# Optimization experiments

Hardware: AMD Instinct MI355X
Metric: run time of the kernel (lower is better)

Reference implementation:

```python
import jax, jax.numpy as jnp
import numpy as np

D_MODEL, D_K, D_V = 1024, 128, 128
B, S = 8, 2048


def setup_inputs() -> dict:
    key = jax.random.key(0)
    ks = jax.random.split(key, 10)
    scale = 1.0 / np.sqrt(D_MODEL)
    return {
        "inputs_q": jax.random.normal(ks[0], (B, S, D_MODEL), jnp.float32),
        "inputs_k": jax.random.normal(ks[1], (B, S, D_MODEL), jnp.float32),
        "inputs_v": jax.random.normal(ks[2], (B, S, D_MODEL), jnp.float32),
        "mask": jax.random.randint(ks[3], (B, 1, S), 0, 2, jnp.int32),
        "Wq": jax.random.normal(ks[4], (D_MODEL, D_K), jnp.float32) * scale,
        "bq": jnp.zeros((D_K,), jnp.float32),
        "Wk": jax.random.normal(ks[5], (D_MODEL, D_K), jnp.float32) * scale,
        "bk": jnp.zeros((D_K,), jnp.float32),
        "Wv": jax.random.normal(ks[6], (D_MODEL, D_V), jnp.float32) * scale,
        "bv": jnp.zeros((D_V,), jnp.float32),
    }


def reference(inputs_q, inputs_k, inputs_v, mask, Wq, bq, Wk, bk, Wv, bv):
    query = inputs_q @ Wq + bq            # [B,Sq,d_k]
    key = inputs_k @ Wk + bk              # [B,Sk,d_k]
    value = inputs_v @ Wv + bv            # [B,Sk,d_v]
    scores = jnp.einsum('bqd,bkd->bqk', query, key) / jnp.sqrt(jnp.float32(D_K))
    # original: mask==True means attend; inverted mask positions get -1e9
    mask_float = jnp.logical_not(mask.astype(bool)).astype(jnp.float32)  # [B,1,Sk]
    scores = scores + mask_float * (-1e9)
    attention_weights = jax.nn.softmax(scores, axis=-1)
    attention_weights = attention_weights * (1.0 - mask_float)
    output = jnp.einsum('bqk,bkv->bqv', attention_weights, value)
    return output
```

## Files before the change

kernel.cpp:

```cpp
#include <hip/hip_runtime.h>

#define L2E 1.44269504088896341f
#define SM_SHIFT 5.77078016355585f

typedef _Float16 h8 __attribute__((ext_vector_type(8)));
typedef float f4 __attribute__((ext_vector_type(4)));

__device__ __forceinline__ void gll16(const void* g, void* l) {
  __builtin_amdgcn_global_load_lds((const __attribute__((address_space(1))) void*)g,
                                   (__attribute__((address_space(3))) void*)l, 16, 0, 0);
}

__device__ __forceinline__ f4 mfma_h(h8 a, h8 b, f4 c) {
  return __builtin_amdgcn_mfma_f32_16x16x32_f16(a, b, c, 0, 0, 0);
}

__device__ __forceinline__ h8 pack8(const float4& a, const float4& b) {
  h8 hv;
  hv[0] = (_Float16)a.x; hv[1] = (_Float16)a.y; hv[2] = (_Float16)a.z; hv[3] = (_Float16)a.w;
  hv[4] = (_Float16)b.x; hv[5] = (_Float16)b.y; hv[6] = (_Float16)b.z; hv[7] = (_Float16)b.w;
  return hv;
}

__global__ void wt_prep(const float* __restrict__ Wq, const float* __restrict__ Wk,
                        const float* __restrict__ Wv, const int* __restrict__ maskp,
                        _Float16* __restrict__ Wt, _Float16* __restrict__ mh) {
  int z = blockIdx.y;
  const float* W = (z == 0) ? Wq : ((z == 1) ? Wk : Wv);
  _Float16* o = Wt + (size_t)z * 131072;
  int idx = blockIdx.x * 256 + threadIdx.x;
  int k = idx >> 7, n = idx & 127;
  o[(k >> 6) * 8192 + ((k >> 3) & 7) * 1024 + n * 8 + (k & 7)] = (_Float16)W[idx];
  if (z == 0 && idx < 16384) mh[idx] = (_Float16)(float)maskp[idx];
}

__global__ __launch_bounds__(256, 3) void proj_qkv(
    const float* __restrict__ Xq, const float* __restrict__ Xk, const float* __restrict__ Xv,
    const _Float16* __restrict__ Wt, const int* __restrict__ maskp,
    const float* __restrict__ bq, const float* __restrict__ bk, const float* __restrict__ bv,
    _Float16* __restrict__ Qh, _Float16* __restrict__ Kpk, _Float16* __restrict__ Vpk) {
  const int z = blockIdx.y;
  const float* X; const float* bias;
  if (z == 0) { X = Xq; bias = bq; }
  else if (z == 1) { X = Xk; bias = bk; }
  else { X = Xv; bias = bv; }
  const _Float16* Wz = Wt + (size_t)z * 131072;
  const int row0 = blockIdx.x * 64;
  const int tid = threadIdx.x;
  const int lane = tid & 63, wid = tid >> 6;
  const int wr = wid >> 1, wc = wid & 1;
  const int l15 = lane & 15, g = lane >> 4;

  __shared__ __align__(16) _Float16 Al[4096];
  __shared__ __align__(16) _Float16 Bl[2][8192];

  f4 acc[2][4];
#pragma unroll
  for (int i = 0; i < 2; i++)
#pragma unroll
    for (int j = 0; j < 4; j++) acc[i][j] = (f4){0.f, 0.f, 0.f, 0.f};

  float4 areg[2][2];
  const int ar_row = tid >> 3, ar_ko = tid & 7;
  auto loadA = [&](int t) {
#pragma unroll
    for (int it = 0; it < 2; it++) {
      const float* gp = X + (size_t)(row0 + it * 32 + ar_row) * 1024 + t * 64 + ar_ko * 8;
      areg[it][0] = *(const float4*)gp;
      areg[it][1] = *(const float4*)(gp + 4);
    }
  };
  auto writeA = [&]() {
#pragma unroll
    for (int it = 0; it < 2; it++) {
      int row = it * 32 + ar_row;
      *(h8*)&Al[(row * 8 + (ar_ko ^ (row & 7))) * 8] = pack8(areg[it][0], areg[it][1]);
    }
  };
  auto loadB = [&](int buf, int t) {
#pragma unroll
    for (int it = 0; it < 4; it++)
      gll16(Wz + t * 8192 + it * 2048 + tid * 8, &Bl[buf][it * 2048 + tid * 8]);
  };
  auto compute = [&](int buf) {
#pragma unroll
    for (int kc = 0; kc < 2; kc++) {
      int o = kc * 4 + g;
      h8 af[2], bf[4];
#pragma unroll
      for (int mf = 0; mf < 2; mf++) {
        int row = wr * 32 + mf * 16 + l15;
        af[mf] = *(const h8*)&Al[(row * 8 + (o ^ (row & 7))) * 8];
      }
#pragma unroll
      for (int nf = 0; nf < 4; nf++) {
        int col = wc * 64 + nf * 16 + l15;
        bf[nf] = *(const h8*)&Bl[buf][(o * 128 + col) * 8];
      }
#pragma unroll
      for (int mf = 0; mf < 2; mf++)
#pragma unroll
        for (int nf = 0; nf < 4; nf++)
          acc[mf][nf] = mfma_h(af[mf], bf[nf], acc[mf][nf]);
    }
  };

  loadA(0);
  loadB(0, 0);

  int cur = 0;
  for (int t = 0; t < 16; t++) {
    writeA();
    __syncthreads();
    if (t < 15) {
      loadA(t + 1);
      loadB(cur ^ 1, t + 1);
    }
    compute(cur);
    __syncthreads();
    cur ^= 1;
  }

  const float qscale = (z == 0) ? 0.08838834764831845f : 1.0f;
#pragma unroll
  for (int nf = 0; nf < 4; nf++) {
    int colb = wc * 64 + nf * 16 + l15;
    float bv_ = bias[colb];
#pragma unroll
    for (int mf = 0; mf < 2; mf++)
#pragma unroll
      for (int jj = 0; jj < 4; jj++) {
        int m = row0 + wr * 32 + mf * 16 + g * 4 + jj;
        float v = (acc[mf][nf][jj] + bv_) * qscale;
        if (z == 2) v *= (float)maskp[m];
        _Float16 hv = (_Float16)v;
        if (z == 0) Qh[m * 128 + colb] = hv;
        else if (z == 1) Kpk[(m >> 6) * 8192 + (colb >> 3) * 512 + (m & 63) * 8 + (colb & 7)] = hv;
        else Vpk[(m >> 6) * 8192 + ((m & 63) >> 3) * 1024 + colb * 8 + (m & 7)] = hv;
      }
  }
}

__global__ __launch_bounds__(256) void attn_fwd(
    const _Float16* __restrict__ Qh, const _Float16* __restrict__ Kpk,
    const _Float16* __restrict__ Vpk, const _Float16* __restrict__ maskh,
    float* __restrict__ Out) {
  const int bi = blockIdx.x & 7;
  const int qt = blockIdx.x >> 3;
  const int tid = threadIdx.x;
  const int lane = tid & 63, wid = tid >> 6;
  const int l15 = lane & 15, g = lane >> 4;

  __shared__ __align__(16) _Float16 Kt[16384];
  __shared__ __align__(16) _Float16 Vt[16384];
  __shared__ __align__(16) _Float16 Pl[4][2048];

  const size_t mb = (size_t)bi * 2048;
  const int q0 = qt * 64 + wid * 16;

  h8 qf[4];
#pragma unroll
  for (int c = 0; c < 4; c++)
    qf[c] = *(const h8*)(Qh + (mb + q0 + l15) * 128 + c * 32 + g * 8);

  const _Float16* Kb = Kpk + (size_t)bi * 262144;
  const _Float16* Vb = Vpk + (size_t)bi * 262144;
  const _Float16* mhp = maskh + mb;

  f4 oacc[8];
#pragma unroll
  for (int i = 0; i < 8; i++) oacc[i] = (f4){0.f, 0.f, 0.f, 0.f};
  f4 lacc = (f4){0.f, 0.f, 0.f, 0.f};

  h8 kreg[8], vreg[8];
#pragma unroll
  for (int it = 0; it < 8; it++) {
    kreg[it] = *(const h8*)(Kb + (it * 256 + tid) * 8);
    vreg[it] = *(const h8*)(Vb + (it * 256 + tid) * 8);
  }

  for (int s = 0; s < 16; s++) {
#pragma unroll
    for (int it = 0; it < 8; it++) {
      int wg = it * 256 + tid;
      *(h8*)&Kt[(wg ^ ((wg >> 6) & 7)) * 8] = kreg[it];
      *(h8*)&Vt[(wg ^ ((wg >> 7) & 7)) * 8] = vreg[it];
    }
    __syncthreads();

    if (s < 15) {
      const _Float16* gk = Kb + (size_t)(s + 1) * 16384;
      const _Float16* gv = Vb + (size_t)(s + 1) * 16384;
#pragma unroll
      for (int it = 0; it < 8; it++) {
        kreg[it] = *(const h8*)(gk + (it * 256 + tid) * 8);
        vreg[it] = *(const h8*)(gv + (it * 256 + tid) * 8);
      }
    }

    f4 sc[8];
#pragma unroll
    for (int nf = 0; nf < 8; nf++) sc[nf] = (f4){0.f, 0.f, 0.f, 0.f};
#pragma unroll
    for (int c = 0; c < 4; c++) {
      int dblk = c * 4 + g;
#pragma unroll
      for (int nf = 0; nf < 8; nf++) {
        int key = nf * 16 + l15;
        int kg = (key >> 6) * 1024 + dblk * 64 + ((key & 63) ^ (dblk & 7));
        h8 bfr = *(const h8*)&Kt[kg * 8];
        sc[nf] = mfma_h(qf[c], bfr, sc[nf]);
      }
    }

#pragma unroll
    for (int nf = 0; nf < 8; nf++) {
      int key = nf * 16 + l15;
      int kb = key >> 3, j = key & 7;
#pragma unroll
      for (int jj = 0; jj < 4; jj++) {
        int q = g * 4 + jj;
        float p = __builtin_amdgcn_exp2f(sc[nf][jj] * L2E - SM_SHIFT);
        Pl[wid][((kb * 16 + (q ^ (kb & 7))) << 3) + j] = (_Float16)p;
      }
    }

#pragma unroll
    for (int kc = 0; kc < 4; kc++) {
      int kb = kc * 4 + g;
      h8 pa = *(const h8*)&Pl[wid][((kb * 16 + (l15 ^ (kb & 7))) << 3)];
      h8 mfr = *(const h8*)(mhp + s * 128 + kc * 32 + g * 8);
      lacc = mfma_h(pa, mfr, lacc);
      int rbl = (kc & 1) * 4 + g;
#pragma unroll
      for (int nf = 0; nf < 8; nf++) {
        int d = nf * 16 + l15;
        int vg = (kc >> 1) * 1024 + rbl * 128 + (d ^ (rbl & 7));
        h8 va = *(const h8*)&Vt[vg * 8];
        oacc[nf] = mfma_h(pa, va, oacc[nf]);
      }
    }
    __syncthreads();
  }

  float inv[4];
#pragma unroll
  for (int jj = 0; jj < 4; jj++)
    inv[jj] = (lacc[jj] > 0.f) ? 1.0f / lacc[jj] : 0.0f;
#pragma unroll
  for (int nf = 0; nf < 8; nf++)
#pragma unroll
    for (int jj = 0; jj < 4; jj++)
      Out[(mb + q0 + g * 4 + jj) * 128 + nf * 16 + l15] = oacc[nf][jj] * inv[jj];
}

extern "C" void kernel_launch(void* const* d_in, const int* in_sizes, int n_in,
                              void* d_out, int out_size, void* d_ws, size_t ws_size,
                              hipStream_t stream) {
  const float* Xq = (const float*)d_in[0];
  const float* Xk = (const float*)d_in[1];
  const float* Xv = (const float*)d_in[2];
  const int* mask = (const int*)d_in[3];
  const float* Wq = (const float*)d_in[4];
  const float* bq = (const float*)d_in[5];
  const float* Wk = (const float*)d_in[6];
  const float* bk = (const float*)d_in[7];
  const float* Wv = (const float*)d_in[8];
  const float* bv = (const float*)d_in[9];
  float* Out = (float*)d_out;

  char* ws = (char*)d_ws;
  _Float16* Qh    = (_Float16*)(ws);
  _Float16* Kpk   = (_Float16*)(ws + 4194304);
  _Float16* Vpk   = (_Float16*)(ws + 8388608);
  _Float16* Wt    = (_Float16*)(ws + 12582912);
  _Float16* maskh = (_Float16*)(ws + 13369344);

  wt_prep<<<dim3(512, 3), 256, 0, stream>>>(Wq, Wk, Wv, mask, Wt, maskh);
  proj_qkv<<<dim3(256, 3), 256, 0, stream>>>(Xq, Xk, Xv, Wt, mask, bq, bk, bv, Qh, Kpk, Vpk);
  attn_fwd<<<dim3(256), 256, 0, stream>>>(Qh, Kpk, Vpk, maskh, Out);
}
```

Baseline: 105.6 us.

## Split attention key tiles across wave pairs and double grid size

Each block now handles 32 queries instead of 64. Its four waves form two query groups by two key halves, and each wave processes 64 of the 128 keys per tile. Partial output and row-sum accumulators are combined through shared memory at the end, and the grid doubles to 512 blocks with launch bounds asking for two blocks per CU. The goal is more parallelism and occupancy on the 256-CU device. In exchange, every K/V tile is loaded by twice as many blocks, which adds global and LDS traffic, and the cross-wave reduction adds a synchronisation step.

```diff
diff --git a/kernel.cpp b/kernel.cpp
--- a/kernel.cpp
+++ b/kernel.cpp
@@ -141,7 +141,7 @@
   }
 }
 
-__global__ __launch_bounds__(256) void attn_fwd(
+__global__ __launch_bounds__(256, 2) void attn_fwd(
     const _Float16* __restrict__ Qh, const _Float16* __restrict__ Kpk,
     const _Float16* __restrict__ Vpk, const _Float16* __restrict__ maskh,
     float* __restrict__ Out) {
@@ -150,13 +150,15 @@
   const int tid = threadIdx.x;
   const int lane = tid & 63, wid = tid >> 6;
   const int l15 = lane & 15, g = lane >> 4;
+  const int qg = wid & 1;
+  const int kh = wid >> 1;
 
   __shared__ __align__(16) _Float16 Kt[16384];
   __shared__ __align__(16) _Float16 Vt[16384];
-  __shared__ __align__(16) _Float16 Pl[4][2048];
+  __shared__ __align__(16) _Float16 Pl[4][1024];
 
   const size_t mb = (size_t)bi * 2048;
-  const int q0 = qt * 64 + wid * 16;
+  const int q0 = qt * 32 + qg * 16;
 
   h8 qf[4];
 #pragma unroll
@@ -198,25 +200,25 @@
       }
     }
 
-    f4 sc[8];
-#pragma unroll
-    for (int nf = 0; nf < 8; nf++) sc[nf] = (f4){0.f, 0.f, 0.f, 0.f};
+    f4 sc[4];
+#pragma unroll
+    for (int nf = 0; nf < 4; nf++) sc[nf] = (f4){0.f, 0.f, 0.f, 0.f};
 #pragma unroll
     for (int c = 0; c < 4; c++) {
       int dblk = c * 4 + g;
 #pragma unroll
-      for (int nf = 0; nf < 8; nf++) {
-        int key = nf * 16 + l15;
-        int kg = (key >> 6) * 1024 + dblk * 64 + ((key & 63) ^ (dblk & 7));
+      for (int nf = 0; nf < 4; nf++) {
+        int key64 = nf * 16 + l15;
+        int kg = kh * 1024 + dblk * 64 + (key64 ^ (dblk & 7));
         h8 bfr = *(const h8*)&Kt[kg * 8];
         sc[nf] = mfma_h(qf[c], bfr, sc[nf]);
       }
     }
 
 #pragma unroll
-    for (int nf = 0; nf < 8; nf++) {
-      int key = nf * 16 + l15;
-      int kb = key >> 3, j = key & 7;
+    for (int nf = 0; nf < 4; nf++) {
+      int key64 = nf * 16 + l15;
+      int kb = key64 >> 3, j = key64 & 7;
 #pragma unroll
       for (int jj = 0; jj < 4; jj++) {
         int q = g * 4 + jj;
@@ -226,16 +228,15 @@
     }
 
 #pragma unroll
-    for (int kc = 0; kc < 4; kc++) {
-      int kb = kc * 4 + g;
-      h8 pa = *(const h8*)&Pl[wid][((kb * 16 + (l15 ^ (kb & 7))) << 3)];
-      h8 mfr = *(const h8*)(mhp + s * 128 + kc * 32 + g * 8);
+    for (int kc2 = 0; kc2 < 2; kc2++) {
+      int kbp = kc2 * 4 + g;
+      h8 pa = *(const h8*)&Pl[wid][((kbp * 16 + (l15 ^ (kbp & 7))) << 3)];
+      h8 mfr = *(const h8*)(mhp + s * 128 + kh * 64 + kc2 * 32 + g * 8);
       lacc = mfma_h(pa, mfr, lacc);
-      int rbl = (kc & 1) * 4 + g;
 #pragma unroll
       for (int nf = 0; nf < 8; nf++) {
         int d = nf * 16 + l15;
-        int vg = (kc >> 1) * 1024 + rbl * 128 + (d ^ (rbl & 7));
+        int vg = kh * 1024 + kbp * 128 + (d ^ (kbp & 7));
         h8 va = *(const h8*)&Vt[vg * 8];
         oacc[nf] = mfma_h(pa, va, oacc[nf]);
       }
@@ -243,15 +244,40 @@
     __syncthreads();
   }
 
-  float inv[4];
-#pragma unroll
-  for (int jj = 0; jj < 4; jj++)
-    inv[jj] = (lacc[jj] > 0.f) ? 1.0f / lacc[jj] : 0.0f;
-#pragma unroll
-  for (int nf = 0; nf < 8; nf++)
+  float* red = (float*)Kt;
+  if (kh == 1) {
+    int base = qg * 2304;
+#pragma unroll
+    for (int nf = 0; nf < 8; nf++)
+#pragma unroll
+      for (int jj = 0; jj < 4; jj++)
+        red[base + (nf * 4 + jj) * 64 + lane] = oacc[nf][jj];
 #pragma unroll
     for (int jj = 0; jj < 4; jj++)
-      Out[(mb + q0 + g * 4 + jj) * 128 + nf * 16 + l15] = oacc[nf][jj] * inv[jj];
+      red[base + 2048 + jj * 64 + lane] = lacc[jj];
+  }
+  __syncthreads();
+  if (kh == 0) {
+    int base = qg * 2304;
+#pragma unroll
+    for (int nf = 0; nf < 8; nf++)
+#pragma unroll
+      for (int jj = 0; jj < 4; jj++)
+        oacc[nf][jj] += red[base + (nf * 4 + jj) * 64 + lane];
+#pragma unroll
+    for (int jj = 0; jj < 4; jj++)
+      lacc[jj] += red[base + 2048 + jj * 64 + lane];
+
+    float inv[4];
+#pragma unroll
+    for (int jj = 0; jj < 4; jj++)
+      inv[jj] = (lacc[jj] > 0.f) ? 1.0f / lacc[jj] : 0.0f;
+#pragma unroll
+    for (int nf = 0; nf < 8; nf++)
+#pragma unroll
+      for (int jj = 0; jj < 4; jj++)
+        Out[(mb + q0 + g * 4 + jj) * 128 + nf * 16 + l15] = oacc[nf][jj] * inv[jj];
+  }
 }
 
 extern "C" void kernel_launch(void* const* d_in, const int* in_sizes, int n_in,
@@ -278,5 +304,5 @@
 
   wt_prep<<<dim3(512, 3), 256, 0, stream>>>(Wq, Wk, Wv, mask, Wt, maskh);
   proj_qkv<<<dim3(256, 3), 256, 0, stream>>>(Xq, Xk, Xv, Wt, mask, bq, bk, bv, Qh, Kpk, Vpk);
-  attn_fwd<<<dim3(256), 256, 0, stream>>>(Qh, Kpk, Vpk, maskh, Out);
-}
+  attn_fwd<<<dim3(512), 256, 0, stream>>>(Qh, Kpk, Vpk, maskh, Out);
+}
```

After: 90.52 us (median of 2 runs). 1.17x faster.
